# Performance work log

Measured on AMD Instinct MI355X. Metric: run time of the kernel, lower is better.

Reference implementation:

```python
import jax, jax.numpy as jnp
import numpy as np


def setup_inputs() -> dict:
    key = jax.random.key(0)
    k1, k2, k3 = jax.random.split(key, 3)
    D, N, K = 512, 131072, 64
    x = jax.random.normal(k1, (D, N), dtype=jnp.float32)
    a_bar = jax.random.uniform(k2, (K, N), dtype=jnp.float32)
    c = jax.random.normal(k3, (K, D), dtype=jnp.float32)
    return {"x": x, "a_bar": a_bar, "c": c}


def reference(x, a_bar, c):
    # V[k, d] = sum_n a_bar[k, n] * (x[d, n] - c[k, d])
    #         = (a_bar @ x.T)[k, d] - c[k, d] * sum_n a_bar[k, n]
    # Fused form: one GEMM + one row-sum, never materializing (K, D, N) residuals.
    ax = jnp.einsum('kn,dn->kd', a_bar, x)        # (K, D)
    a_sum = jnp.sum(a_bar, axis=1, keepdims=True)  # (K, 1)
    V = ax - c * a_sum                              # (K, D)
    return V
```

## Files before the change

### kernel.cpp

```cpp
#include <hip/hip_runtime.h>
#include <hip/hip_bf16.h>


#define K_ROWS 64
#define D_COLS 512
#define N_RED  131072LL
#define TOTAL_STEPS 4096
#define ABUF 4096

typedef __attribute__((ext_vector_type(8))) short short8;
typedef __attribute__((ext_vector_type(4))) float f32x4;

static __device__ __forceinline__ short f2bf(float f) {
    __bf16 h = (__bf16)f;
    return __builtin_bit_cast(short, h);
}
static __device__ __forceinline__ float bf2f(unsigned short u) {
    return __builtin_bit_cast(float, (unsigned)u << 16);
}
static __device__ __forceinline__ short8 cvt8(float4 a, float4 b) {
    short8 r;
    r[0] = f2bf(a.x); r[1] = f2bf(a.y); r[2] = f2bf(a.z); r[3] = f2bf(a.w);
    r[4] = f2bf(b.x); r[5] = f2bf(b.y); r[6] = f2bf(b.z); r[7] = f2bf(b.w);
    return r;
}

__global__ __launch_bounds__(512, 6) void vlad_stage1(
    const float* __restrict__ x, const float* __restrict__ ab,
    unsigned short* __restrict__ pax, float* __restrict__ pasum, int S)
{
    __shared__ __align__(16) char smem[3][ABUF];

    const int bid = blockIdx.x;
    const int x7  = bid & 7;
    const int g   = (bid >> 3) & 3;
    const int m   = bid >> 5;
    const int s   = m * 8 + x7;
    const int tid = threadIdx.x;
    const int w   = tid >> 6, l = tid & 63, lr = l & 15, lg = l >> 4;
    const int d0  = g * 128;

    const int st0 = (int)(((long long)s       * TOTAL_STEPS) / S);
    const int st1 = (int)(((long long)(s + 1) * TOTAL_STEPS) / S);

    const float* gx = x + (size_t)(d0 + w * 16 + lr) * N_RED + lg * 8;

    const bool at  = (tid < 256);
    const int arow = tid >> 2, aq = tid & 3;
    const float* ga = ab + (size_t)arow * N_RED + aq * 8;
    const int awoff = arow * 64 + ((aq ^ (arow & 3)) << 4);

    const int swz = lr & 3;
    int fa[4];
    #pragma unroll
    for (int t = 0; t < 4; ++t)
        fa[t] = (t * 16 + lr) * 64 + ((lg ^ swz) << 4);

    f32x4 acc[4] = {};
    float asum = 0.f;
    float4 X0, X1, A0, A1, B0, B1;

    if (at) { const float* q = ga + (size_t)st0 * 32; A0 = *(const float4*)q; A1 = *(const float4*)(q + 4); }
    { const float* p = gx + (size_t)st0 * 32; X0 = *(const float4*)p; X1 = *(const float4*)(p + 4); }
    if (at) {
        *(short8*)(smem[0] + awoff) = cvt8(A0, A1);
        asum += ((A0.x + A0.y) + (A0.z + A0.w)) + ((A1.x + A1.y) + (A1.z + A1.w));
    }
    if (at && st0 + 1 < st1) { const float* q = ga + (size_t)(st0 + 1) * 32; A0 = *(const float4*)q; A1 = *(const float4*)(q + 4); }

    int rb = 0;
    #pragma unroll 1
    for (int it = st0; it < st1; ++it) {
        __syncthreads();
        if (at && it + 2 < st1) {
            const float* q = ga + (size_t)(it + 2) * 32;
            B0 = *(const float4*)q; B1 = *(const float4*)(q + 4);
        }
        short8 xf = cvt8(X0, X1);
        if (it + 1 < st1) {
            const float* p = gx + (size_t)(it + 1) * 32;
            X0 = *(const float4*)p; X1 = *(const float4*)(p + 4);
        }

        const char* b = smem[rb];
        short8 a0f = *(const short8*)(b + fa[0]);
        short8 a1f = *(const short8*)(b + fa[1]);
        short8 a2f = *(const short8*)(b + fa[2]);
        short8 a3f = *(const short8*)(b + fa[3]);
        acc[0] = __builtin_amdgcn_mfma_f32_16x16x32_bf16(a0f, xf, acc[0], 0, 0, 0);
        acc[1] = __builtin_amdgcn_mfma_f32_16x16x32_bf16(a1f, xf, acc[1], 0, 0, 0);
        acc[2] = __builtin_amdgcn_mfma_f32_16x16x32_bf16(a2f, xf, acc[2], 0, 0, 0);
        acc[3] = __builtin_amdgcn_mfma_f32_16x16x32_bf16(a3f, xf, acc[3], 0, 0, 0);

        if (at && it + 1 < st1) {
            int wb_ = (rb + 1 == 3) ? 0 : rb + 1;
            *(short8*)(smem[wb_] + awoff) = cvt8(A0, A1);
            asum += ((A0.x + A0.y) + (A0.z + A0.w)) + ((A1.x + A1.y) + (A1.z + A1.w));
            A0 = B0; A1 = B1;
        }
        rb = (rb + 1 == 3) ? 0 : rb + 1;
    }

    unsigned short* dst = pax + (size_t)s * (K_ROWS * D_COLS);
    #pragma unroll
    for (int t = 0; t < 4; ++t)
        #pragma unroll
        for (int r = 0; r < 4; ++r)
            dst[(((g * 8 + w) * 4 + t) * 4 + r) * 64 + l] =
                (unsigned short)f2bf(acc[t][r]);

    if (g == 0 && at) {
        asum += __shfl_xor(asum, 1, 64);
        asum += __shfl_xor(asum, 2, 64);
        if (aq == 0) pasum[s * K_ROWS + arow] = asum;
    }
}

__global__ __launch_bounds__(256) void vlad_stage2(
    const unsigned short* __restrict__ pax, const float* __restrict__ pasum,
    const float* __restrict__ c, float* __restrict__ out, int S)
{
    __shared__ float red[256];
    __shared__ float ared[256];
    const int t  = threadIdx.x;
    const int fo = t & 63;
    const int sp = t >> 6;
    const int fb = blockIdx.x * 64;
    const int f  = fb + fo;

    float acc = 0.f;
    for (int s = sp; s < S; s += 4)
        acc += bf2f(pax[(size_t)s * (K_ROWS * D_COLS) + f]);
    red[t] = acc;

    const int R = (fb >> 6) & 3, T = (fb >> 8) & 3;
    const int ka = T * 16 + (t & 3) * 4 + R;
    float pa = 0.f;
    for (int s2 = t >> 2; s2 < S; s2 += 64)
        pa += pasum[s2 * K_ROWS + ka];
    ared[t] = pa;
    __syncthreads();

    for (int st = 128; st >= 4; st >>= 1) {
        if (t < st) ared[t] += ared[t + st];
        __syncthreads();
    }
    if (sp == 0) {
        const int lr = f & 15, lg = (f >> 4) & 3;
        const int r  = (f >> 6) & 3, tt = (f >> 8) & 3;
        const int w  = (f >> 10) & 7, gg = (f >> 13) & 3;
        const int k  = tt * 16 + lg * 4 + r;
        const int d  = gg * 128 + w * 16 + lr;
        float v = red[t] + red[t + 64] + red[t + 128] + red[t + 192];
        out[k * D_COLS + d] = v - c[k * D_COLS + d] * ared[lg];
    }
}

extern "C" void kernel_launch(void* const* d_in, const int* in_sizes, int n_in,
                              void* d_out, int out_size, void* d_ws, size_t ws_size,
                              hipStream_t stream)
{
    const float* x  = (const float*)d_in[0];
    const float* ab = (const float*)d_in[1];
    const float* c  = (const float*)d_in[2];
    float* out = (float*)d_out;

    int S = 192;
    while (S > 24 &&
           (size_t)S * ((size_t)K_ROWS * D_COLS * 2 + K_ROWS * 4) > ws_size)
        S >>= 1;

    unsigned short* pax = (unsigned short*)d_ws;
    float* pasum = (float*)((char*)d_ws + (size_t)S * K_ROWS * D_COLS * 2);

    vlad_stage1<<<dim3(4 * S), dim3(512), 0, stream>>>(x, ab, pax, pasum, S);
    vlad_stage2<<<dim3((K_ROWS * D_COLS) / 64), dim3(256), 0, stream>>>(pax, pasum, c, out, S);
}
```

Before: 74.03 us.

## Stage x and a_bar through LDS with async global_load_lds triple buffering

Stage1 now loads fp32 x and a_bar tiles straight from global memory into LDS with global_load_lds, using a three-deep pipeline paced by explicit vmcnt waits and barriers. Previously x went through registers and only a_bar used LDS. The bf16 conversion moves to after the LDS read, and the a_sum partial is now computed from LDS by the g==0 blocks. Split count S drops from 192 to 128, and occupancy is lowered to 4 blocks per CU to make room for the larger LDS footprint. The aim is to hide global latency and cut register pressure, at the cost of more LDS traffic and an extra barrier per step.

```diff
diff --git a/kernel.cpp b/kernel.cpp
--- a/kernel.cpp
+++ b/kernel.cpp
@@ -5,8 +5,11 @@
 #define K_ROWS 64
 #define D_COLS 512
 #define N_RED  131072LL
-#define TOTAL_STEPS 4096
-#define ABUF 4096
+
+#define XW     6144
+#define ABASE  49152
+#define ABUF   8192
+#define SMEMSZ 73728
 
 typedef __attribute__((ext_vector_type(8))) short short8;
 typedef __attribute__((ext_vector_type(4))) float f32x4;
@@ -24,12 +27,17 @@
     r[4] = f2bf(b.x); r[5] = f2bf(b.y); r[6] = f2bf(b.z); r[7] = f2bf(b.w);
     return r;
 }
+static __device__ __forceinline__ void gload16(const float* g, char* l) {
+    __builtin_amdgcn_global_load_lds(
+        (const __attribute__((address_space(1))) void*)g,
+        (__attribute__((address_space(3))) void*)l, 16, 0, 0);
+}
 
-__global__ __launch_bounds__(512, 6) void vlad_stage1(
+__global__ __launch_bounds__(512, 4) void vlad_stage1(
     const float* __restrict__ x, const float* __restrict__ ab,
     unsigned short* __restrict__ pax, float* __restrict__ pasum, int S)
 {
-    __shared__ __align__(16) char smem[3][ABUF];
+    __shared__ __align__(16) char smem[SMEMSZ];
 
     const int bid = blockIdx.x;
     const int x7  = bid & 7;
@@ -40,65 +48,68 @@
     const int w   = tid >> 6, l = tid & 63, lr = l & 15, lg = l >> 4;
     const int d0  = g * 128;
 
-    const int st0 = (int)(((long long)s       * TOTAL_STEPS) / S);
-    const int st1 = (int)(((long long)(s + 1) * TOTAL_STEPS) / S);
+    const int chunk = (int)(N_RED / S);
+    const int nst   = chunk >> 5;
+    const size_t nblk = (size_t)s * chunk;
 
-    const float* gx = x + (size_t)(d0 + w * 16 + lr) * N_RED + lg * 8;
+    const int csrc = (((l & 7) ^ (l >> 3)) << 2);
+    const float* gx0 = x + (size_t)(d0 + w * 16 + (l >> 3)) * N_RED + nblk + csrc;
+    const float* gx1 = gx0 + (size_t)8 * N_RED;
+    const float* ga  = ab + (size_t)(w * 8 + (l >> 3)) * N_RED + nblk + csrc;
 
-    const bool at  = (tid < 256);
-    const int arow = tid >> 2, aq = tid & 3;
-    const float* ga = ab + (size_t)arow * N_RED + aq * 8;
-    const int awoff = arow * 64 + ((aq ^ (arow & 3)) << 4);
-
-    const int swz = lr & 3;
-    int fa[4];
+    const int swz = lr & 7;
+    int fx[2], fa[4][2];
     #pragma unroll
-    for (int t = 0; t < 4; ++t)
-        fa[t] = (t * 16 + lr) * 64 + ((lg ^ swz) << 4);
+    for (int h = 0; h < 2; ++h) {
+        fx[h] = lr * 128 + (((lg * 2 + h) ^ swz) << 4);
+        #pragma unroll
+        for (int t = 0; t < 4; ++t)
+            fa[t][h] = (t * 16 + lr) * 128 + (((lg * 2 + h) ^ swz) << 4);
+    }
 
     f32x4 acc[4] = {};
     float asum = 0.f;
-    float4 X0, X1, A0, A1, B0, B1;
+    const bool g0 = (g == 0);
 
-    if (at) { const float* q = ga + (size_t)st0 * 32; A0 = *(const float4*)q; A1 = *(const float4*)(q + 4); }
-    { const float* p = gx + (size_t)st0 * 32; X0 = *(const float4*)p; X1 = *(const float4*)(p + 4); }
-    if (at) {
-        *(short8*)(smem[0] + awoff) = cvt8(A0, A1);
-        asum += ((A0.x + A0.y) + (A0.z + A0.w)) + ((A1.x + A1.y) + (A1.z + A1.w));
-    }
-    if (at && st0 + 1 < st1) { const float* q = ga + (size_t)(st0 + 1) * 32; A0 = *(const float4*)q; A1 = *(const float4*)(q + 4); }
+    auto issue = [&](int it) {
+        const int buf = it % 3;
+        char* xd = smem + w * XW + buf * 2048;
+        gload16(gx0 + (size_t)it * 32, xd);
+        gload16(gx1 + (size_t)it * 32, xd + 1024);
+        gload16(ga  + (size_t)it * 32, smem + ABASE + buf * ABUF + w * 1024);
+    };
 
-    int rb = 0;
+    issue(0);
+    if (nst > 1) issue(1);
+
+    int buf = 0;
     #pragma unroll 1
-    for (int it = st0; it < st1; ++it) {
-        __syncthreads();
-        if (at && it + 2 < st1) {
-            const float* q = ga + (size_t)(it + 2) * 32;
-            B0 = *(const float4*)q; B1 = *(const float4*)(q + 4);
+    for (int it = 0; it < nst; ++it) {
+        if (it + 2 < nst) issue(it + 2);
+        if (it + 2 < nst)      asm volatile("s_waitcnt vmcnt(6)\ns_barrier" ::: "memory");
+        else if (it + 1 < nst) asm volatile("s_waitcnt vmcnt(3)\ns_barrier" ::: "memory");
+        else                   asm volatile("s_waitcnt vmcnt(0)\ns_barrier" ::: "memory");
+
+        const char* bx = smem + w * XW + buf * 2048;
+        const char* ba = smem + ABASE + buf * ABUF;
+
+        float4 xl = *(const float4*)(bx + fx[0]);
+        float4 xh = *(const float4*)(bx + fx[1]);
+        short8 xf = cvt8(xl, xh);
+        #pragma unroll
+        for (int t = 0; t < 4; ++t) {
+            float4 al = *(const float4*)(ba + fa[t][0]);
+            float4 ah = *(const float4*)(ba + fa[t][1]);
+            acc[t] = __builtin_amdgcn_mfma_f32_16x16x32_bf16(
+                         cvt8(al, ah), xf, acc[t], 0, 0, 0);
         }
-        short8 xf = cvt8(X0, X1);
-        if (it + 1 < st1) {
-            const float* p = gx + (size_t)(it + 1) * 32;
-            X0 = *(const float4*)p; X1 = *(const float4*)(p + 4);
+        if (g0) {
+            float4 av = *(const float4*)(ba + tid * 16);
+            asum += (av.x + av.y) + (av.z + av.w);
         }
 
-        const char* b = smem[rb];
-        short8 a0f = *(const short8*)(b + fa[0]);
-        short8 a1f = *(const short8*)(b + fa[1]);
-        short8 a2f = *(const short8*)(b + fa[2]);
-        short8 a3f = *(const short8*)(b + fa[3]);
-        acc[0] = __builtin_amdgcn_mfma_f32_16x16x32_bf16(a0f, xf, acc[0], 0, 0, 0);
-        acc[1] = __builtin_amdgcn_mfma_f32_16x16x32_bf16(a1f, xf, acc[1], 0, 0, 0);
-        acc[2] = __builtin_amdgcn_mfma_f32_16x16x32_bf16(a2f, xf, acc[2], 0, 0, 0);
-        acc[3] = __builtin_amdgcn_mfma_f32_16x16x32_bf16(a3f, xf, acc[3], 0, 0, 0);
-
-        if (at && it + 1 < st1) {
-            int wb_ = (rb + 1 == 3) ? 0 : rb + 1;
-            *(short8*)(smem[wb_] + awoff) = cvt8(A0, A1);
-            asum += ((A0.x + A0.y) + (A0.z + A0.w)) + ((A1.x + A1.y) + (A1.z + A1.w));
-            A0 = B0; A1 = B1;
-        }
-        rb = (rb + 1 == 3) ? 0 : rb + 1;
+        asm volatile("s_waitcnt lgkmcnt(0)\ns_barrier" ::: "memory");
+        buf = (buf + 1 == 3) ? 0 : buf + 1;
     }
 
     unsigned short* dst = pax + (size_t)s * (K_ROWS * D_COLS);
@@ -109,10 +120,11 @@
             dst[(((g * 8 + w) * 4 + t) * 4 + r) * 64 + l] =
                 (unsigned short)f2bf(acc[t][r]);
 
-    if (g == 0 && at) {
+    if (g0) {
         asum += __shfl_xor(asum, 1, 64);
         asum += __shfl_xor(asum, 2, 64);
-        if (aq == 0) pasum[s * K_ROWS + arow] = asum;
+        asum += __shfl_xor(asum, 4, 64);
+        if ((tid & 7) == 0) pasum[s * K_ROWS + (tid >> 3)] = asum;
     }
 }
 
@@ -165,8 +177,8 @@
     const float* c  = (const float*)d_in[2];
     float* out = (float*)d_out;
 
-    int S = 192;
-    while (S > 24 &&
+    int S = 128;
+    while (S > 8 &&
            (size_t)S * ((size_t)K_ROWS * D_COLS * 2 + K_ROWS * 4) > ws_size)
         S >>= 1;
 
```

After: 77.95 us. 5.3% more time.
